# Optimization experiments

Measured on AMD Instinct MI355X. Metric: run time of the kernel, lower is better.

Reference implementation:

```python
import jax, jax.numpy as jnp
import numpy as np

B, T, C = 4, 2048, 768
H, KVH, D = 6, 6, 128
HALF = D // 2


def setup_inputs() -> dict:
    key = jax.random.key(0)
    ks = jax.random.split(key, 5)
    x = jax.random.normal(ks[0], (B, T, C), dtype=jnp.float32)
    # true rotary frequencies
    inv_freq = 1.0 / (10000.0 ** (jnp.arange(HALF, dtype=jnp.float32) / HALF))
    ang = jnp.arange(T, dtype=jnp.float32)[:, None] * inv_freq[None, :]  # [T, HALF]
    cos, sin = jnp.cos(ang), jnp.sin(ang)
    s = 0.02
    wq = jax.random.normal(ks[1], (H * D, C), dtype=jnp.float32) * s
    wk = jax.random.normal(ks[2], (KVH * D, C), dtype=jnp.float32) * s
    wv = jax.random.normal(ks[3], (KVH * D, C), dtype=jnp.float32) * s
    wproj = jax.random.normal(ks[4], (C, C), dtype=jnp.float32) * s
    return {"x": x, "cos": cos, "sin": sin, "wq": wq, "wk": wk, "wv": wv, "wproj": wproj}


def _norm(t, eps=1e-6):
    # torch: (x - mean) / (std + eps), std unbiased (ddof=1)
    mean = jnp.mean(t, axis=-1, keepdims=True)
    var = jnp.sum((t - mean) ** 2, axis=-1, keepdims=True) / (t.shape[-1] - 1)
    return (t - mean) / (jnp.sqrt(var) + eps)


def _rope(t, cos, sin):
    # t: [B, T, heads, D]; cos/sin: [T, HALF]
    x1, x2 = t[..., :HALF], t[..., HALF:]
    c = cos[None, :, None, :]
    s = sin[None, :, None, :]
    return jnp.concatenate([x1 * c + x2 * s, -x1 * s + x2 * c], axis=-1)


def reference(x, cos, sin, wq, wk, wv, wproj):
    q = jnp.einsum('btc,oc->bto', x, wq).reshape(B, T, H, D)
    k = jnp.einsum('btc,oc->bto', x, wk).reshape(B, T, KVH, D)
    v = jnp.einsum('btc,oc->bto', x, wv).reshape(B, T, KVH, D)
    q = _norm(_rope(q, cos, sin))
    k = _norm(_rope(k, cos, sin))
    # -> [B, heads, T, D]
    q = q.transpose(0, 2, 1, 3)
    k = k.transpose(0, 2, 1, 3)
    v = v.transpose(0, 2, 1, 3)
    # nrep = H // KVH == 1, repeat_kv is a no-op here
    scale = 1.0 / jnp.sqrt(jnp.float32(D))
    scores = jnp.einsum('bhtd,bhsd->bhts', q, k) * scale  # [B,H,T,T]
    causal = jnp.tril(jnp.ones((T, T), dtype=bool))
    scores = jnp.where(causal[None, None], scores, jnp.float32(-1e30))
    attn = jax.nn.softmax(scores, axis=-1)
    y = jnp.einsum('bhts,bhsd->bhtd', attn, v)
    y = y.transpose(0, 2, 1, 3).reshape(B, T, H * D)
    return jnp.einsum('bto,co->btc', y, wproj)
```

## Files before the change

### kernel.cpp

```cpp
#include <hip/hip_runtime.h>

#define BB 4
#define TT 2048
#define CC 768
#define HH 6
#define DD 128
#define BT (BB * TT)
#define HALF 64
#define NBH (BB * HH)
#define QKSCALE 0.12753785627919282f

typedef __bf16 v8bf __attribute__((ext_vector_type(8)));
typedef float f32x4 __attribute__((ext_vector_type(4)));

#if __has_builtin(__builtin_amdgcn_exp2f)
#define EXP2(x) __builtin_amdgcn_exp2f(x)
#else
#define EXP2(x) exp2f(x)
#endif

__device__ __forceinline__ unsigned short f2b(float f) {
  union { float f; unsigned u; } v; v.f = f;
  unsigned r = v.u + 0x7FFFu + ((v.u >> 16) & 1u);
  return (unsigned short)(r >> 16);
}
__device__ __forceinline__ float b2f(unsigned short u) {
  union { unsigned u; float f; } v; v.u = (unsigned)u << 16;
  return v.f;
}
__device__ __forceinline__ unsigned pk2(float f0, float f1) {
  union { float f; unsigned u; } a, b; a.f = f1; b.f = f0;
  return __builtin_amdgcn_perm(a.u, b.u, 0x07060302u);
}

__device__ __forceinline__ void load_lds16(const void* g, void* l) {
  __builtin_amdgcn_global_load_lds(
      (const __attribute__((address_space(1))) unsigned int*)g,
      (__attribute__((address_space(3))) unsigned int*)(unsigned int)(unsigned long long)(l),
      16, 0, 0);
}

__global__ __launch_bounds__(256) void cvt_f2b_kernel(const float* __restrict__ src,
                                                      unsigned short* __restrict__ dst,
                                                      int n4) {
  int i = blockIdx.x * 256 + threadIdx.x;
  if (i >= n4) return;
  float4 f = ((const float4*)src)[i];
  ushort4 o;
  o.x = f2b(f.x); o.y = f2b(f.y); o.z = f2b(f.z); o.w = f2b(f.w);
  ((ushort4*)dst)[i] = o;
}

__global__ __launch_bounds__(256) void cvt_w4_kernel(const float* __restrict__ w0,
                                                     const float* __restrict__ w1,
                                                     const float* __restrict__ w2,
                                                     const float* __restrict__ w3,
                                                     unsigned short* __restrict__ dst) {
  int bsel = blockIdx.x / 576;
  int i = (blockIdx.x % 576) * 256 + threadIdx.x;
  const float* src = bsel == 0 ? w0 : bsel == 1 ? w1 : bsel == 2 ? w2 : w3;
  float4 f = ((const float4*)src)[i];
  ushort4 o;
  o.x = f2b(f.x); o.y = f2b(f.y); o.z = f2b(f.z); o.w = f2b(f.w);
  ((ushort4*)(dst + bsel * 589824))[i] = o;
}

__global__ __launch_bounds__(256) void gemm_qkv(const unsigned short* __restrict__ A,
                                                const unsigned short* __restrict__ Wall,
                                                unsigned short* __restrict__ qb,
                                                unsigned short* __restrict__ kb,
                                                unsigned short* __restrict__ vt) {
  __shared__ __align__(16) unsigned short As[2][512 * 8];
  __shared__ __align__(16) unsigned short Bs[2][512 * 8];
  const int m0 = blockIdx.x * 128;
  const int wsel = blockIdx.y / HH, h = blockIdx.y % HH;
  const unsigned short* W = Wall + (size_t)wsel * 589824 + (size_t)h * 128 * CC;
  const int tid = threadIdx.x;
  const int wave = tid >> 6, lane = tid & 63;
  const int fr = lane & 15, quad = lane >> 4;
  const int wm = (wave & 1) * 64, wn = (wave >> 1) * 64;

  f32x4 acc[4][4];
#pragma unroll
  for (int i = 0; i < 4; i++)
#pragma unroll
    for (int j = 0; j < 4; j++) acc[i][j] = (f32x4){0.f, 0.f, 0.f, 0.f};

  auto stage = [&](int kk, int buf) {
#pragma unroll
    for (int it = 0; it < 2; it++) {
      int base_slot = wave * 128 + it * 64;
      int sigma = base_slot + lane;
      int r = sigma >> 2, g = (sigma & 3) ^ ((r >> 1) & 3);
      load_lds16(A + (size_t)(m0 + r) * CC + kk + g * 8, &As[buf][base_slot * 8]);
      load_lds16(W + (size_t)r * CC + kk + g * 8, &Bs[buf][base_slot * 8]);
    }
  };

  stage(0, 0);
  __syncthreads();
  for (int step = 0; step < CC / 32; step++) {
    int buf = step & 1;
    if (step + 1 < CC / 32) stage((step + 1) * 32, buf ^ 1);
    v8bf af[4], bfr[4];
#pragma unroll
    for (int i = 0; i < 4; i++) {
      int ra = wm + i * 16 + fr;
      af[i] = *(const v8bf*)&As[buf][(4 * ra + (quad ^ ((ra >> 1) & 3))) * 8];
      int rb = wn + i * 16 + fr;
      bfr[i] = *(const v8bf*)&Bs[buf][(4 * rb + (quad ^ ((rb >> 1) & 3))) * 8];
    }
#pragma unroll
    for (int i = 0; i < 4; i++)
#pragma unroll
      for (int j = 0; j < 4; j++)
        acc[i][j] = __builtin_amdgcn_mfma_f32_16x16x32_bf16(af[i], bfr[j], acc[i][j], 0, 0, 0);
    __syncthreads();
  }

  if (wsel < 2) {
    unsigned short* dst = wsel ? kb : qb;
#pragma unroll
    for (int i = 0; i < 4; i++) {
      int rr0 = m0 + wm + i * 16 + quad * 4;
      int b = rr0 >> 11, t0 = rr0 & 2047;
      size_t base = ((size_t)(b * HH + h) * TT + t0) * DD;
#pragma unroll
      for (int j = 0; j < 4; j++) {
        int d = wn + j * 16 + fr;
#pragma unroll
        for (int r = 0; r < 4; r++)
          dst[base + (size_t)r * DD + d] = f2b(acc[i][j][r]);
      }
    }
  } else {
#pragma unroll
    for (int i = 0; i < 4; i++) {
      int rr0 = m0 + wm + i * 16 + quad * 4;
      int b = rr0 >> 11, t0 = rr0 & 2047;
      int bh = b * HH + h;
#pragma unroll
      for (int j = 0; j < 4; j++) {
        int d = wn + j * 16 + fr;
        ushort4 u = { f2b(acc[i][j][0]), f2b(acc[i][j][1]),
                      f2b(acc[i][j][2]), f2b(acc[i][j][3]) };
        *(ushort4*)&vt[((size_t)bh * DD + d) * TT + t0] = u;
      }
    }
  }
}

__global__ __launch_bounds__(256) void gemm_w64(const unsigned short* __restrict__ A,
                                                const unsigned short* __restrict__ W,
                                                float* __restrict__ C) {
  __shared__ __align__(16) unsigned short As[2][256 * 8];
  __shared__ __align__(16) unsigned short Bs[2][512 * 8];
  const int m0 = blockIdx.x * 64, n0 = blockIdx.y * 128;
  const int tid = threadIdx.x;
  const int wave = tid >> 6, lane = tid & 63;
  const int fr = lane & 15, quad = lane >> 4;
  const int wm = (wave & 1) * 32, wn = (wave >> 1) * 64;

  f32x4 acc[2][4];
#pragma unroll
  for (int i = 0; i < 2; i++)
#pragma unroll
    for (int j = 0; j < 4; j++) acc[i][j] = (f32x4){0.f, 0.f, 0.f, 0.f};

  auto stage = [&](int kk, int buf) {
    {
      int base_slot = wave * 64;
      int sigma = base_slot + lane;
      int r = sigma >> 2, g = (sigma & 3) ^ ((r >> 1) & 3);
      load_lds16(A + (size_t)(m0 + r) * CC + kk + g * 8, &As[buf][base_slot * 8]);
    }
#pragma unroll
    for (int it = 0; it < 2; it++) {
      int base_slot = wave * 128 + it * 64;
      int sigma = base_slot + lane;
      int r = sigma >> 2, g = (sigma & 3) ^ ((r >> 1) & 3);
      load_lds16(W + (size_t)(n0 + r) * CC + kk + g * 8, &Bs[buf][base_slot * 8]);
    }
  };

  stage(0, 0);
  __syncthreads();
  for (int step = 0; step < CC / 32; step++) {
    int buf = step & 1;
    if (step + 1 < CC / 32) stage((step + 1) * 32, buf ^ 1);
    v8bf af[2], bfr[4];
#pragma unroll
    for (int i = 0; i < 2; i++) {
      int ra = wm + i * 16 + fr;
      af[i] = *(const v8bf*)&As[buf][(4 * ra + (quad ^ ((ra >> 1) & 3))) * 8];
    }
#pragma unroll
    for (int j = 0; j < 4; j++) {
      int rb = wn + j * 16 + fr;
      bfr[j] = *(const v8bf*)&Bs[buf][(4 * rb + (quad ^ ((rb >> 1) & 3))) * 8];
    }
#pragma unroll
    for (int i = 0; i < 2; i++)
#pragma unroll
      for (int j = 0; j < 4; j++)
        acc[i][j] = __builtin_amdgcn_mfma_f32_16x16x32_bf16(af[i], bfr[j], acc[i][j], 0, 0, 0);
    __syncthreads();
  }

  const int orow = m0 + wm + quad * 4;
#pragma unroll
  for (int i = 0; i < 2; i++)
#pragma unroll
    for (int j = 0; j < 4; j++) {
      int oc = n0 + wn + j * 16 + fr;
#pragma unroll
      for (int r = 0; r < 4; r++)
        C[(size_t)(orow + i * 16 + r) * CC + oc] = acc[i][j][r];
    }
}

__global__ __launch_bounds__(256) void rope_norm_kernel(unsigned short* __restrict__ qk,
                                                        const float* __restrict__ cosb,
                                                        const float* __restrict__ sinb,
                                                        float scale) {
  int idx = blockIdx.x * 4 + (threadIdx.x >> 6);
  int lane = threadIdx.x & 63;
  int tpos = idx & (TT - 1);
  size_t base = (size_t)idx * DD;

  float x1 = b2f(qk[base + lane]);
  float x2 = b2f(qk[base + HALF + lane]);
  float c = cosb[tpos * HALF + lane];
  float s = sinb[tpos * HALF + lane];
  float o1 = x1 * c + x2 * s;
  float o2 = x2 * c - x1 * s;

  float sum = o1 + o2;
#pragma unroll
  for (int off = 32; off; off >>= 1) sum += __shfl_xor(sum, off);
  float mean = sum * (1.f / 128.f);
  float d1 = o1 - mean, d2 = o2 - mean;
  float vs = d1 * d1 + d2 * d2;
#pragma unroll
  for (int off = 32; off; off >>= 1) vs += __shfl_xor(vs, off);
  float inv = scale / (sqrtf(vs * (1.f / 127.f)) + 1e-6f);

  qk[base + lane] = f2b(d1 * inv);
  qk[base + HALF + lane] = f2b(d2 * inv);
}

__global__ __launch_bounds__(256) void attn_mfma(const unsigned short* __restrict__ qtb,
                                                 const unsigned short* __restrict__ ktb,
                                                 const unsigned short* __restrict__ vtb,
                                                 unsigned short* __restrict__ Opart,
                                                 float* __restrict__ lpart) {
  __shared__ __align__(16) unsigned short Ks[2][512 * 8];
  __shared__ __align__(16) unsigned short Vts[2][512 * 8];
  __shared__ __align__(16) unsigned short Ps[4][16][40];

  const int u = blockIdx.x;
  const int bh = u % NBH;
  const int uu = u / NBH;
  int qt, c;
  if (uu < 32)      { qt = 31 - (uu >> 2);        c = uu & 3; }
  else if (uu < 56) { int k = uu - 32; int q3 = k / 3; qt = 23 - q3; c = k - q3 * 3; }
  else if (uu < 72) { int k = uu - 56; qt = 15 - (k >> 1); c = k & 1; }
  else              { qt = 7 - (uu - 72);         c = 0; }
  const int t0 = c * 16;
  const int t1 = min(t0 + 16, 2 * qt + 2);
  const int niter = t1 - t0;

  const int tid = threadIdx.x;
  const int wave = tid >> 6, lane = tid & 63;
  const int fr = lane & 15, quad = lane >> 4;
  const size_t head_base = (size_t)bh * TT * DD;
  const int m0 = qt * 64 + wave * 16;

  v8bf qf[4];
#pragma unroll
  for (int kbk = 0; kbk < 4; kbk++)
    qf[kbk] = *(const v8bf*)(qtb + head_base + (size_t)(m0 + fr) * DD + kbk * 32 + quad * 8);

  const __bf16 one_bf = (__bf16)1.0f;
  v8bf ones = {one_bf, one_bf, one_bf, one_bf, one_bf, one_bf, one_bf, one_bf};

  f32x4 oacc[8];
#pragma unroll
  for (int i = 0; i < 8; i++) oacc[i] = (f32x4){0.f, 0.f, 0.f, 0.f};
  f32x4 lacc = (f32x4){0.f, 0.f, 0.f, 0.f};

  auto stage = [&](int jt, int buf) {
    const unsigned short* kbase = ktb + head_base + (size_t)(jt * 32) * DD;
    const unsigned short* vbase = vtb + head_base + jt * 32;
#pragma unroll
    for (int it = 0; it < 2; it++) {
      int base_slot = it * 256 + wave * 64;
      int sigma = base_slot + lane;
      int s = sigma >> 4, gk = (sigma & 15) ^ (s & 7);
      load_lds16(kbase + (size_t)s * DD + gk * 8, &Ks[buf][base_slot * 8]);
      int d = sigma >> 2, gv = (sigma & 3) ^ ((d >> 1) & 3);
      load_lds16(vbase + (size_t)d * TT + gv * 8, &Vts[buf][base_slot * 8]);
    }
  };

  stage(t0, 0);
  __syncthreads();

  for (int it = 0; it < niter; it++) {
    const int jt = t0 + it;
    const int buf = it & 1;
    if (it + 1 < niter) stage(jt + 1, buf ^ 1);

    const int j0 = jt * 32;
    if (j0 <= m0 + 15) {
      f32x4 st0 = (f32x4){0.f, 0.f, 0.f, 0.f}, st1 = (f32x4){0.f, 0.f, 0.f, 0.f};
#pragma unroll
      for (int kbk = 0; kbk < 4; kbk++) {
        int g = 4 * kbk + quad;
        v8bf a0 = *(const v8bf*)&Ks[buf][(16 * fr + (g ^ (fr & 7))) * 8];
        v8bf a1 = *(const v8bf*)&Ks[buf][(16 * (fr + 16) + (g ^ (fr & 7))) * 8];
        st0 = __builtin_amdgcn_mfma_f32_16x16x32_bf16(a0, qf[kbk], st0, 0, 0, 0);
        st1 = __builtin_amdgcn_mfma_f32_16x16x32_bf16(a1, qf[kbk], st1, 0, 0, 0);
      }

      float p[8];
      if (j0 + 31 > m0) {
        const int qrow = m0 + fr;
#pragma unroll
        for (int r = 0; r < 4; r++) {
          int c0 = j0 + quad * 4 + r;
          p[r]     = (c0      <= qrow) ? EXP2(st0[r]) : 0.f;
          p[4 + r] = (c0 + 16 <= qrow) ? EXP2(st1[r]) : 0.f;
        }
      } else {
#pragma unroll
        for (int r = 0; r < 4; r++) { p[r] = EXP2(st0[r]); p[4 + r] = EXP2(st1[r]); }
      }
      uint2 w0 = { pk2(p[0], p[1]), pk2(p[2], p[3]) };
      uint2 w1 = { pk2(p[4], p[5]), pk2(p[6], p[7]) };
      *(uint2*)&Ps[wave][fr][quad * 4] = w0;
      *(uint2*)&Ps[wave][fr][16 + quad * 4] = w1;

      v8bf pa = *(const v8bf*)&Ps[wave][fr][quad * 8];
#pragma unroll
      for (int nt2 = 0; nt2 < 8; nt2++) {
        int d = nt2 * 16 + fr;
        v8bf vb = *(const v8bf*)&Vts[buf][(4 * d + (quad ^ ((d >> 1) & 3))) * 8];
        oacc[nt2] = __builtin_amdgcn_mfma_f32_16x16x32_bf16(pa, vb, oacc[nt2], 0, 0, 0);
      }
      lacc = __builtin_amdgcn_mfma_f32_16x16x32_bf16(pa, ones, lacc, 0, 0, 0);
    }
    __syncthreads();
  }

  unsigned short* Oc = Opart + (size_t)c * (NBH * TT * DD) + head_base;
#pragma unroll
  for (int nt2 = 0; nt2 < 8; nt2++)
#pragma unroll
    for (int r = 0; r < 4; r++)
      Oc[(size_t)(m0 + quad * 4 + r) * DD + nt2 * 16 + fr] = f2b(oacc[nt2][r]);
  if (fr == 0) {
#pragma unroll
    for (int r = 0; r < 4; r++)
      lpart[c * (NBH * TT) + bh * TT + m0 + quad * 4 + r] = lacc[r];
  }
}

__global__ __launch_bounds__(256) void combine_kernel(const unsigned short* __restrict__ Opart,
                                                      const float* __restrict__ lpart,
                                                      unsigned short* __restrict__ yb) {
  int idx = blockIdx.x * 256 + threadIdx.x;
  int row = idx >> 5;
  int dg = (idx & 31) * 4;
  int t = row & 2047;
  int qt = t >> 6;
  int nc = (2 * qt + 2 + 15) >> 4;

  float a0 = 0.f, a1 = 0.f, a2 = 0.f, a3 = 0.f, l = 0.f;
  for (int cchunk = 0; cchunk < nc; cchunk++) {
    ushort4 o = *(const ushort4*)&Opart[(size_t)cchunk * (NBH * TT * DD) + (size_t)row * DD + dg];
    a0 += b2f(o.x); a1 += b2f(o.y); a2 += b2f(o.z); a3 += b2f(o.w);
    l += lpart[cchunk * (NBH * TT) + row];
  }
  float linv = 1.f / l;
  int bh = row >> 11;
  int b = bh / HH, h = bh % HH;
  ushort4 u = { f2b(a0 * linv), f2b(a1 * linv), f2b(a2 * linv), f2b(a3 * linv) };
  *(ushort4*)&yb[((size_t)(b * TT + t)) * CC + h * DD + dg] = u;
}

extern "C" void kernel_launch(void* const* d_in, const int* in_sizes, int n_in,
                              void* d_out, int out_size, void* d_ws, size_t ws_size,
                              hipStream_t stream) {
  const float* x     = (const float*)d_in[0];
  const float* cosb  = (const float*)d_in[1];
  const float* sinb  = (const float*)d_in[2];
  const float* wq    = (const float*)d_in[3];
  const float* wk    = (const float*)d_in[4];
  const float* wv    = (const float*)d_in[5];
  const float* wproj = (const float*)d_in[6];
  float* out = (float*)d_out;

  char* w = (char*)d_ws;
  unsigned short* q_t   = (unsigned short*)(w);
  unsigned short* k_t   = (unsigned short*)(w + 12582912);
  unsigned short* v_t   = (unsigned short*)(w + 25165824);
  unsigned short* yb    = (unsigned short*)(w + 37748736);
  unsigned short* xb    = (unsigned short*)(w + 50331648);
  float*          lpart = (float*)(w + 50331648);
  unsigned short* wb    = (unsigned short*)(w + 62914560);
  unsigned short* Opart = (unsigned short*)(w + 67633152);

  const int nx4 = BT * CC / 4;

  cvt_f2b_kernel<<<nx4 / 256, 256, 0, stream>>>(x, xb, nx4);
  cvt_w4_kernel<<<2304, 256, 0, stream>>>(wq, wk, wv, wproj, wb);

  gemm_qkv<<<dim3(BT / 128, 3 * HH), 256, 0, stream>>>(xb, wb, q_t, k_t, v_t);

  int nvec = NBH * TT;
  rope_norm_kernel<<<nvec / 4, 256, 0, stream>>>(q_t, cosb, sinb, QKSCALE);
  rope_norm_kernel<<<nvec / 4, 256, 0, stream>>>(k_t, cosb, sinb, 1.0f);

  attn_mfma<<<1920, 256, 0, stream>>>(q_t, k_t, v_t, Opart, lpart);
  combine_kernel<<<6144, 256, 0, stream>>>(Opart, lpart, yb);

  gemm_w64<<<dim3(BT / 64, CC / 128), 256, 0, stream>>>(yb, wb + 3 * 589824, out);
}
```

Baseline: 246.8 us.

## Double attention query tile per wave and merge conversion and rope launches

```diff
diff --git a/kernel.cpp b/kernel.cpp
--- a/kernel.cpp
+++ b/kernel.cpp
@@ -13,12 +13,6 @@
 typedef __bf16 v8bf __attribute__((ext_vector_type(8)));
 typedef float f32x4 __attribute__((ext_vector_type(4)));
 
-#if __has_builtin(__builtin_amdgcn_exp2f)
-#define EXP2(x) __builtin_amdgcn_exp2f(x)
-#else
-#define EXP2(x) exp2f(x)
-#endif
-
 __device__ __forceinline__ unsigned short f2b(float f) {
   union { float f; unsigned u; } v; v.f = f;
   unsigned r = v.u + 0x7FFFu + ((v.u >> 16) & 1u);
@@ -40,29 +34,29 @@
       16, 0, 0);
 }
 
-__global__ __launch_bounds__(256) void cvt_f2b_kernel(const float* __restrict__ src,
-                                                      unsigned short* __restrict__ dst,
-                                                      int n4) {
-  int i = blockIdx.x * 256 + threadIdx.x;
-  if (i >= n4) return;
+__global__ __launch_bounds__(256) void cvt_all_kernel(const float* __restrict__ x,
+                                                      const float* __restrict__ w0,
+                                                      const float* __restrict__ w1,
+                                                      const float* __restrict__ w2,
+                                                      const float* __restrict__ w3,
+                                                      unsigned short* __restrict__ xb,
+                                                      unsigned short* __restrict__ wb) {
+  int bx = blockIdx.x;
+  const float* src;
+  unsigned short* dst;
+  int i;
+  if (bx < 6144) {
+    src = x; dst = xb; i = bx * 256 + threadIdx.x;
+  } else {
+    int bsel = (bx - 6144) / 576;
+    src = bsel == 0 ? w0 : bsel == 1 ? w1 : bsel == 2 ? w2 : w3;
+    dst = wb + bsel * 589824;
+    i = ((bx - 6144) % 576) * 256 + threadIdx.x;
+  }
   float4 f = ((const float4*)src)[i];
   ushort4 o;
   o.x = f2b(f.x); o.y = f2b(f.y); o.z = f2b(f.z); o.w = f2b(f.w);
   ((ushort4*)dst)[i] = o;
-}
-
-__global__ __launch_bounds__(256) void cvt_w4_kernel(const float* __restrict__ w0,
-                                                     const float* __restrict__ w1,
-                                                     const float* __restrict__ w2,
-                                                     const float* __restrict__ w3,
-                                                     unsigned short* __restrict__ dst) {
-  int bsel = blockIdx.x / 576;
-  int i = (blockIdx.x % 576) * 256 + threadIdx.x;
-  const float* src = bsel == 0 ? w0 : bsel == 1 ? w1 : bsel == 2 ? w2 : w3;
-  float4 f = ((const float4*)src)[i];
-  ushort4 o;
-  o.x = f2b(f.x); o.y = f2b(f.y); o.z = f2b(f.z); o.w = f2b(f.w);
-  ((ushort4*)(dst + bsel * 589824))[i] = o;
 }
 
 __global__ __launch_bounds__(256) void gemm_qkv(const unsigned short* __restrict__ A,
@@ -219,11 +213,14 @@
     }
 }
 
-__global__ __launch_bounds__(256) void rope_norm_kernel(unsigned short* __restrict__ qk,
-                                                        const float* __restrict__ cosb,
-                                                        const float* __restrict__ sinb,
-                                                        float scale) {
-  int idx = blockIdx.x * 4 + (threadIdx.x >> 6);
+__global__ __launch_bounds__(256) void rope_all_kernel(unsigned short* __restrict__ qb,
+                                                       unsigned short* __restrict__ kb,
+                                                       const float* __restrict__ cosb,
+                                                       const float* __restrict__ sinb) {
+  int bx = blockIdx.x;
+  unsigned short* qk = (bx < 12288) ? qb : kb;
+  float scale = (bx < 12288) ? QKSCALE : 1.0f;
+  int idx = (bx % 12288) * 4 + (threadIdx.x >> 6);
   int lane = threadIdx.x & 63;
   int tpos = idx & (TT - 1);
   size_t base = (size_t)idx * DD;
@@ -256,38 +253,43 @@
                                                  float* __restrict__ lpart) {
   __shared__ __align__(16) unsigned short Ks[2][512 * 8];
   __shared__ __align__(16) unsigned short Vts[2][512 * 8];
-  __shared__ __align__(16) unsigned short Ps[4][16][40];
+  __shared__ __align__(16) unsigned short Ps[4][32][40];
 
   const int u = blockIdx.x;
   const int bh = u % NBH;
   const int uu = u / NBH;
   int qt, c;
-  if (uu < 32)      { qt = 31 - (uu >> 2);        c = uu & 3; }
-  else if (uu < 56) { int k = uu - 32; int q3 = k / 3; qt = 23 - q3; c = k - q3 * 3; }
-  else if (uu < 72) { int k = uu - 56; qt = 15 - (k >> 1); c = k & 1; }
-  else              { qt = 7 - (uu - 72);         c = 0; }
+  if (uu < 16)      { qt = 15 - (uu >> 2); c = uu & 3; }
+  else if (uu < 28) { int k = uu - 16; int q3 = k / 3; qt = 11 - q3; c = k - q3 * 3; }
+  else if (uu < 36) { int k = uu - 28; qt = 7 - (k >> 1); c = k & 1; }
+  else              { qt = 3 - (uu - 36); c = 0; }
   const int t0 = c * 16;
-  const int t1 = min(t0 + 16, 2 * qt + 2);
+  const int t1 = min(t0 + 16, 4 * qt + 4);
   const int niter = t1 - t0;
 
   const int tid = threadIdx.x;
   const int wave = tid >> 6, lane = tid & 63;
   const int fr = lane & 15, quad = lane >> 4;
   const size_t head_base = (size_t)bh * TT * DD;
-  const int m0 = qt * 64 + wave * 16;
-
-  v8bf qf[4];
-#pragma unroll
-  for (int kbk = 0; kbk < 4; kbk++)
-    qf[kbk] = *(const v8bf*)(qtb + head_base + (size_t)(m0 + fr) * DD + kbk * 32 + quad * 8);
+  const int m0 = qt * 128 + wave * 32;
+
+  v8bf qf[2][4];
+#pragma unroll
+  for (int qs = 0; qs < 2; qs++)
+#pragma unroll
+    for (int kbk = 0; kbk < 4; kbk++)
+      qf[qs][kbk] = *(const v8bf*)(qtb + head_base +
+                                   (size_t)(m0 + qs * 16 + fr) * DD + kbk * 32 + quad * 8);
 
   const __bf16 one_bf = (__bf16)1.0f;
   v8bf ones = {one_bf, one_bf, one_bf, one_bf, one_bf, one_bf, one_bf, one_bf};
 
-  f32x4 oacc[8];
-#pragma unroll
-  for (int i = 0; i < 8; i++) oacc[i] = (f32x4){0.f, 0.f, 0.f, 0.f};
-  f32x4 lacc = (f32x4){0.f, 0.f, 0.f, 0.f};
+  f32x4 oacc[2][8];
+#pragma unroll
+  for (int qs = 0; qs < 2; qs++)
+#pragma unroll
+    for (int i = 0; i < 8; i++) oacc[qs][i] = (f32x4){0.f, 0.f, 0.f, 0.f};
+  f32x4 lacc[2] = {(f32x4){0.f, 0.f, 0.f, 0.f}, (f32x4){0.f, 0.f, 0.f, 0.f}};
 
   auto stage = [&](int jt, int buf) {
     const unsigned short* kbase = ktb + head_base + (size_t)(jt * 32) * DD;
@@ -312,57 +314,71 @@
     if (it + 1 < niter) stage(jt + 1, buf ^ 1);
 
     const int j0 = jt * 32;
-    if (j0 <= m0 + 15) {
-      f32x4 st0 = (f32x4){0.f, 0.f, 0.f, 0.f}, st1 = (f32x4){0.f, 0.f, 0.f, 0.f};
+    if (j0 <= m0 + 31) {
+      f32x4 st[2][2];
+#pragma unroll
+      for (int qs = 0; qs < 2; qs++) { st[qs][0] = (f32x4){0,0,0,0}; st[qs][1] = (f32x4){0,0,0,0}; }
 #pragma unroll
       for (int kbk = 0; kbk < 4; kbk++) {
         int g = 4 * kbk + quad;
         v8bf a0 = *(const v8bf*)&Ks[buf][(16 * fr + (g ^ (fr & 7))) * 8];
         v8bf a1 = *(const v8bf*)&Ks[buf][(16 * (fr + 16) + (g ^ (fr & 7))) * 8];
-        st0 = __builtin_amdgcn_mfma_f32_16x16x32_bf16(a0, qf[kbk], st0, 0, 0, 0);
-        st1 = __builtin_amdgcn_mfma_f32_16x16x32_bf16(a1, qf[kbk], st1, 0, 0, 0);
+        st[0][0] = __builtin_amdgcn_mfma_f32_16x16x32_bf16(a0, qf[0][kbk], st[0][0], 0, 0, 0);
+        st[0][1] = __builtin_amdgcn_mfma_f32_16x16x32_bf16(a1, qf[0][kbk], st[0][1], 0, 0, 0);
+        st[1][0] = __builtin_amdgcn_mfma_f32_16x16x32_bf16(a0, qf[1][kbk], st[1][0], 0, 0, 0);
+        st[1][1] = __builtin_amdgcn_mfma_f32_16x16x32_bf16(a1, qf[1][kbk], st[1][1], 0, 0, 0);
       }
 
-      float p[8];
-      if (j0 + 31 > m0) {
-        const int qrow = m0 + fr;
-#pragma unroll
-        for (int r = 0; r < 4; r++) {
-          int c0 = j0 + quad * 4 + r;
-          p[r]     = (c0      <= qrow) ? EXP2(st0[r]) : 0.f;
-          p[4 + r] = (c0 + 16 <= qrow) ? EXP2(st1[r]) : 0.f;
+      const bool diag = (j0 + 31 > m0);
+#pragma unroll
+      for (int qs = 0; qs < 2; qs++) {
+        float p[8];
+        if (diag) {
+          const int qrow = m0 + qs * 16 + fr;
+#pragma unroll
+          for (int r = 0; r < 4; r++) {
+            int c0 = j0 + quad * 4 + r;
+            p[r]     = (c0      <= qrow) ? exp2f(st[qs][0][r]) : 0.f;
+            p[4 + r] = (c0 + 16 <= qrow) ? exp2f(st[qs][1][r]) : 0.f;
+          }
+        } else {
+#pragma unroll
+          for (int r = 0; r < 4; r++) { p[r] = exp2f(st[qs][0][r]); p[4 + r] = exp2f(st[qs][1][r]); }
         }
-      } else {
-#pragma unroll
-        for (int r = 0; r < 4; r++) { p[r] = EXP2(st0[r]); p[4 + r] = EXP2(st1[r]); }
+        uint2 w0 = { pk2(p[0], p[1]), pk2(p[2], p[3]) };
+        uint2 w1 = { pk2(p[4], p[5]), pk2(p[6], p[7]) };
+        *(uint2*)&Ps[wave][qs * 16 + fr][quad * 4] = w0;
+        *(uint2*)&Ps[wave][qs * 16 + fr][16 + quad * 4] = w1;
       }
-      uint2 w0 = { pk2(p[0], p[1]), pk2(p[2], p[3]) };
-      uint2 w1 = { pk2(p[4], p[5]), pk2(p[6], p[7]) };
-      *(uint2*)&Ps[wave][fr][quad * 4] = w0;
-      *(uint2*)&Ps[wave][fr][16 + quad * 4] = w1;
-
-      v8bf pa = *(const v8bf*)&Ps[wave][fr][quad * 8];
+
+      v8bf pa0 = *(const v8bf*)&Ps[wave][fr][quad * 8];
+      v8bf pa1 = *(const v8bf*)&Ps[wave][16 + fr][quad * 8];
 #pragma unroll
       for (int nt2 = 0; nt2 < 8; nt2++) {
         int d = nt2 * 16 + fr;
         v8bf vb = *(const v8bf*)&Vts[buf][(4 * d + (quad ^ ((d >> 1) & 3))) * 8];
-        oacc[nt2] = __builtin_amdgcn_mfma_f32_16x16x32_bf16(pa, vb, oacc[nt2], 0, 0, 0);
+        oacc[0][nt2] = __builtin_amdgcn_mfma_f32_16x16x32_bf16(pa0, vb, oacc[0][nt2], 0, 0, 0);
+        oacc[1][nt2] = __builtin_amdgcn_mfma_f32_16x16x32_bf16(pa1, vb, oacc[1][nt2], 0, 0, 0);
       }
-      lacc = __builtin_amdgcn_mfma_f32_16x16x32_bf16(pa, ones, lacc, 0, 0, 0);
+      lacc[0] = __builtin_amdgcn_mfma_f32_16x16x32_bf16(pa0, ones, lacc[0], 0, 0, 0);
+      lacc[1] = __builtin_amdgcn_mfma_f32_16x16x32_bf16(pa1, ones, lacc[1], 0, 0, 0);
     }
     __syncthreads();
   }
 
   unsigned short* Oc = Opart + (size_t)c * (NBH * TT * DD) + head_base;
 #pragma unroll
-  for (int nt2 = 0; nt2 < 8; nt2++)
-#pragma unroll
-    for (int r = 0; r < 4; r++)
-      Oc[(size_t)(m0 + quad * 4 + r) * DD + nt2 * 16 + fr] = f2b(oacc[nt2][r]);
-  if (fr == 0) {
-#pragma unroll
-    for (int r = 0; r < 4; r++)
-      lpart[c * (NBH * TT) + bh * TT + m0 + quad * 4 + r] = lacc[r];
+  for (int qs = 0; qs < 2; qs++) {
+#pragma unroll
+    for (int nt2 = 0; nt2 < 8; nt2++)
+#pragma unroll
+      for (int r = 0; r < 4; r++)
+        Oc[(size_t)(m0 + qs * 16 + quad * 4 + r) * DD + nt2 * 16 + fr] = f2b(oacc[qs][nt2][r]);
+    if (fr == 0) {
+#pragma unroll
+      for (int r = 0; r < 4; r++)
+        lpart[c * (NBH * TT) + bh * TT + m0 + qs * 16 + quad * 4 + r] = lacc[qs][r];
+    }
   }
 }
 
@@ -373,8 +389,8 @@
   int row = idx >> 5;
   int dg = (idx & 31) * 4;
   int t = row & 2047;
-  int qt = t >> 6;
-  int nc = (2 * qt + 2 + 15) >> 4;
+  int qt = t >> 7;
+  int nc = (4 * qt + 4 + 15) >> 4;
 
   float a0 = 0.f, a1 = 0.f, a2 = 0.f, a3 = 0.f, l = 0.f;
   for (int cchunk = 0; cchunk < nc; cchunk++) {
@@ -411,18 +427,13 @@
   unsigned short* wb    = (unsigned short*)(w + 62914560);
   unsigned short* Opart = (unsigned short*)(w + 67633152);
 
-  const int nx4 = BT * CC / 4;
-
-  cvt_f2b_kernel<<<nx4 / 256, 256, 0, stream>>>(x, xb, nx4);
-  cvt_w4_kernel<<<2304, 256, 0, stream>>>(wq, wk, wv, wproj, wb);
+  cvt_all_kernel<<<8448, 256, 0, stream>>>(x, wq, wk, wv, wproj, xb, wb);
 
   gemm_qkv<<<dim3(BT / 128, 3 * HH), 256, 0, stream>>>(xb, wb, q_t, k_t, v_t);
 
-  int nvec = NBH * TT;
-  rope_norm_kernel<<<nvec / 4, 256, 0, stream>>>(q_t, cosb, sinb, QKSCALE);
-  rope_norm_kernel<<<nvec / 4, 256, 0, stream>>>(k_t, cosb, sinb, 1.0f);
-
-  attn_mfma<<<1920, 256, 0, stream>>>(q_t, k_t, v_t, Opart, lpart);
+  rope_all_kernel<<<24576, 256, 0, stream>>>(q_t, k_t, cosb, sinb);
+
+  attn_mfma<<<960, 256, 0, stream>>>(q_t, k_t, v_t, Opart, lpart);
   combine_kernel<<<6144, 256, 0, stream>>>(Opart, lpart, yb);
 
   gemm_w64<<<dim3(BT / 64, CC / 128), 256, 0, stream>>>(yb, wb + 3 * 589824, out);
```

Result: no change. 244.4 us (-1.0%).
